# Performance work log

Hardware: AMD Instinct MI355X
Metric: run time of the kernel (lower is better)

## Reference

```python
import jax, jax.numpy as jnp
import numpy as np

N_HEADS = 16
ROPE_BASE = 10000.0


def _rope_tables(T, head_dim, dtype):
    d2 = head_dim // 2
    inv_freq = 1.0 / (ROPE_BASE ** (jnp.arange(0, head_dim, 2, dtype=jnp.float32) / head_dim))
    t = jnp.arange(T, dtype=jnp.float32)
    freqs = jnp.outer(t, inv_freq)  # [T, d2]
    cos = jnp.cos(freqs)[None, :, None, :].astype(dtype)  # [1,T,1,d2]
    sin = jnp.sin(freqs)[None, :, None, :].astype(dtype)
    return cos, sin


def _apply_rotary(x, cos, sin):
    # x: [B,T,H,D]; rotate halves
    d = x.shape[-1] // 2
    x1, x2 = x[..., :d], x[..., d:]
    return jnp.concatenate([x1 * cos + x2 * sin, -x1 * sin + x2 * cos], axis=-1)


def setup_inputs() -> dict:
    key = jax.random.key(0)
    k1, k2, k3 = jax.random.split(key, 3)
    B, T, C = 2, 2048, 1024
    x = jax.random.normal(k1, (B, T, C), dtype=jnp.float32)
    w_attn = jax.random.normal(k2, (3 * C, C), dtype=jnp.float32) * (1.0 / np.sqrt(C))
    w_proj = jax.random.normal(k3, (C, C), dtype=jnp.float32) * (1.0 / np.sqrt(C))
    return {"x": x, "w_attn": w_attn, "w_proj": w_proj}


def reference(x, w_attn, w_proj):
    B, T, C = x.shape
    H = N_HEADS
    D = C // H
    qkv = jnp.einsum('btc,fc->btf', x, w_attn)  # [B,T,3C]
    q, k, v = jnp.split(qkv, 3, axis=2)
    q = q.reshape(B, T, H, D)
    k = k.reshape(B, T, H, D)
    v = v.reshape(B, T, H, D)
    cos, sin = _rope_tables(T, D, x.dtype)
    q = _apply_rotary(q, cos, sin)
    k = _apply_rotary(k, cos, sin)
    # causal SDPA, scale 1/sqrt(D)
    scale = 1.0 / np.sqrt(D)
    scores = jnp.einsum('bqhd,bkhd->bhqk', q, k) * scale
    causal = jnp.tril(jnp.ones((T, T), dtype=bool))
    scores = jnp.where(causal[None, None], scores, jnp.finfo(scores.dtype).min)
    attn = jax.nn.softmax(scores, axis=-1)
    y = jnp.einsum('bhqk,bkhd->bqhd', attn, v).reshape(B, T, C)
    return jnp.einsum('btc,oc->bto', y, w_proj)
```

## Files before the change

### kernel.cpp

```cpp
#include <hip/hip_runtime.h>
#include <math.h>

typedef __bf16 bf16x8 __attribute__((ext_vector_type(8)));
typedef float f32x4 __attribute__((ext_vector_type(4)));

__device__ __forceinline__ unsigned f2bf(float f) {
    union { float f; unsigned u; } v; v.f = f;
    return (v.u + 0x7FFFu + ((v.u >> 16) & 1u)) >> 16;
}

__device__ __forceinline__ unsigned cvtpk(float a, float b) {
    unsigned r;
    __asm__("v_cvt_pk_bf16_f32 %0, %1, %2" : "=v"(r) : "v"(a), "v"(b));
    return r;
}

__device__ __forceinline__ void gload16(const ushort* g, ushort* l) {
    __builtin_amdgcn_global_load_lds(
        (const __attribute__((address_space(1))) void*)g,
        (__attribute__((address_space(3))) void*)l, 16, 0, 0);
}

__device__ __forceinline__ bool src_is_fp32(const unsigned* s) {
    int sane = 0;
#pragma unroll
    for (int i = 0; i < 64; ++i) {
        unsigned lo = s[i] & 0xFFFFu;
        unsigned e = (lo >> 7) & 0xFF;
        if (lo == 0u || (e >= 100u && e <= 140u)) sane++;
    }
    return sane < 48;
}

__global__ __launch_bounds__(256) void tobf16_all_kernel(
    const unsigned* __restrict__ s0, const unsigned* __restrict__ s1,
    const unsigned* __restrict__ s2,
    ushort* __restrict__ d0, ushort* __restrict__ d1, ushort* __restrict__ d2) {
    const int bx = blockIdx.x;
    const unsigned* src;
    ushort* dst;
    int lb;
    if (bx < 2048)      { src = s0; dst = d0; lb = bx; }
    else if (bx < 3584) { src = s1; dst = d1; lb = bx - 2048; }
    else                { src = s2; dst = d2; lb = bx - 3584; }
    const int i = lb * 2048 + threadIdx.x * 8;
    if (src_is_fp32(src)) {
        const float* fs = (const float*)src;
        float4 f0 = *(const float4*)(fs + i);
        float4 f1 = *(const float4*)(fs + i + 4);
        uint4 o;
        o.x = f2bf(f0.x) | (f2bf(f0.y) << 16);
        o.y = f2bf(f0.z) | (f2bf(f0.w) << 16);
        o.z = f2bf(f1.x) | (f2bf(f1.y) << 16);
        o.w = f2bf(f1.z) | (f2bf(f1.w) << 16);
        *(uint4*)(dst + i) = o;
    } else {
        *(uint4*)(dst + i) = *(const uint4*)((const ushort*)src + i);
    }
}

constexpr int GBM = 128, GBN = 128, GBK = 32;

__global__ __launch_bounds__(256) void gemm_qkv_rope_kernel(
    const ushort* __restrict__ A, const ushort* __restrict__ Bmat,
    ushort* __restrict__ qkvh, int K) {
    __shared__ ushort As[2][GBM * GBK];
    __shared__ ushort Bs[2][GBN * GBK];

    const int tid  = threadIdx.x;
    const int lane = tid & 63;
    const int wv   = tid >> 6;
    const int wm   = (wv >> 1) * 64;
    const int wn   = (wv & 1) * 64;

    const ushort* Ab = A + (size_t)blockIdx.x * GBM * K;
    const ushort* Bb = Bmat + (size_t)blockIdx.y * GBN * K;

    f32x4 acc[4][4];
#pragma unroll
    for (int i = 0; i < 4; i++)
#pragma unroll
        for (int j = 0; j < 4; j++) acc[i][j] = (f32x4){0.f, 0.f, 0.f, 0.f};

    const int srow = tid >> 2;
    const int scol = (tid & 3) * 8;
    const int fr = lane & 15;
    const int fk = (lane >> 4) * 8;
    const int nK = K >> 5;

    gload16(Ab + (size_t)srow * K + scol,        As[0] + wv * 512);
    gload16(Ab + (size_t)(srow + 64) * K + scol, As[0] + wv * 512 + 2048);
    gload16(Bb + (size_t)srow * K + scol,        Bs[0] + wv * 512);
    gload16(Bb + (size_t)(srow + 64) * K + scol, Bs[0] + wv * 512 + 2048);

#pragma unroll 1
    for (int it = 0; it < nK; ++it) {
        const int cur = it & 1;
        __syncthreads();
        if (it + 1 < nK) {
            const int k0 = (it + 1) << 5, nxt = cur ^ 1;
            gload16(Ab + (size_t)srow * K + k0 + scol,        As[nxt] + wv * 512);
            gload16(Ab + (size_t)(srow + 64) * K + k0 + scol, As[nxt] + wv * 512 + 2048);
            gload16(Bb + (size_t)srow * K + k0 + scol,        Bs[nxt] + wv * 512);
            gload16(Bb + (size_t)(srow + 64) * K + k0 + scol, Bs[nxt] + wv * 512 + 2048);
        }
        bf16x8 af[4], bfr[4];
#pragma unroll
        for (int i = 0; i < 4; i++)
            af[i] = *(const bf16x8*)(As[cur] + (wm + i * 16 + fr) * GBK + fk);
#pragma unroll
        for (int j = 0; j < 4; j++)
            bfr[j] = *(const bf16x8*)(Bs[cur] + (wn + j * 16 + fr) * GBK + fk);
#pragma unroll
        for (int i = 0; i < 4; i++)
#pragma unroll
            for (int j = 0; j < 4; j++)
                acc[i][j] = __builtin_amdgcn_mfma_f32_16x16x32_bf16(af[i], bfr[j], acc[i][j], 0, 0, 0);
    }

    const int crow0 = (lane >> 4) * 4;
    const int col0  = blockIdx.y * GBN + wn;
    const int which = col0 >> 10;
    const int hh    = (col0 >> 6) & 15;
    ushort* outp = qkvh + (size_t)which * 4194304 + (size_t)hh * 131072;

    if (which < 2) {
        const float inva = exp2f((float)fr * -0.41524101186f);
        const float invb = exp2f((float)(fr + 16) * -0.41524101186f);
        const float qs = (which == 0) ? 0.125f : 1.0f;
#pragma unroll
        for (int i = 0; i < 4; i++)
#pragma unroll
            for (int r = 0; r < 4; r++) {
                int row = blockIdx.x * GBM + wm + i * 16 + crow0 + r;
                int t = row & 2047;
                size_t ob = ((size_t)(row >> 11)) * 2097152 + (size_t)t * 64;
                float sa, ca, sb, cb;
                __sincosf((float)t * inva, &sa, &ca);
                __sincosf((float)t * invb, &sb, &cb);
                float q0 = acc[i][0][r], q1 = acc[i][1][r];
                float q2 = acc[i][2][r], q3 = acc[i][3][r];
                float n0 = (q0 * ca + q2 * sa) * qs;
                float n1 = (q1 * cb + q3 * sb) * qs;
                float n2 = (q2 * ca - q0 * sa) * qs;
                float n3 = (q3 * cb - q1 * sb) * qs;
                unsigned u01 = cvtpk(n0, n1);
                unsigned u23 = cvtpk(n2, n3);
                outp[ob + fr]      = (ushort)(u01 & 0xFFFFu);
                outp[ob + 16 + fr] = (ushort)(u01 >> 16);
                outp[ob + 32 + fr] = (ushort)(u23 & 0xFFFFu);
                outp[ob + 48 + fr] = (ushort)(u23 >> 16);
            }
    } else {
#pragma unroll
        for (int i = 0; i < 4; i++)
#pragma unroll
            for (int r = 0; r < 4; r++) {
                int row = blockIdx.x * GBM + wm + i * 16 + crow0 + r;
                int t = row & 2047;
                size_t ob = ((size_t)(row >> 11)) * 2097152 + (size_t)t * 64;
                unsigned u01 = cvtpk(acc[i][0][r], acc[i][1][r]);
                unsigned u23 = cvtpk(acc[i][2][r], acc[i][3][r]);
                outp[ob + fr]      = (ushort)(u01 & 0xFFFFu);
                outp[ob + 16 + fr] = (ushort)(u01 >> 16);
                outp[ob + 32 + fr] = (ushort)(u23 & 0xFFFFu);
                outp[ob + 48 + fr] = (ushort)(u23 >> 16);
            }
    }
}

__global__ __launch_bounds__(256) void gemm_bt_kernel(
    const ushort* __restrict__ A, const ushort* __restrict__ Bmat,
    float* __restrict__ C, int M, int N, int K) {
    __shared__ ushort As[2][GBM * GBK];
    __shared__ ushort Bs[2][GBN * GBK];

    const int tid  = threadIdx.x;
    const int lane = tid & 63;
    const int wv   = tid >> 6;
    const int wm   = (wv >> 1) * 64;
    const int wn   = (wv & 1) * 64;

    const ushort* Ab = A + (size_t)blockIdx.x * GBM * K;
    const ushort* Bb = Bmat + (size_t)blockIdx.y * GBN * K;

    f32x4 acc[4][4];
#pragma unroll
    for (int i = 0; i < 4; i++)
#pragma unroll
        for (int j = 0; j < 4; j++) acc[i][j] = (f32x4){0.f, 0.f, 0.f, 0.f};

    const int srow = tid >> 2;
    const int scol = (tid & 3) * 8;
    const int fr = lane & 15;
    const int fk = (lane >> 4) * 8;
    const int nK = K >> 5;

    gload16(Ab + (size_t)srow * K + scol,        As[0] + wv * 512);
    gload16(Ab + (size_t)(srow + 64) * K + scol, As[0] + wv * 512 + 2048);
    gload16(Bb + (size_t)srow * K + scol,        Bs[0] + wv * 512);
    gload16(Bb + (size_t)(srow + 64) * K + scol, Bs[0] + wv * 512 + 2048);

#pragma unroll 1
    for (int it = 0; it < nK; ++it) {
        const int cur = it & 1;
        __syncthreads();
        if (it + 1 < nK) {
            const int k0 = (it + 1) << 5, nxt = cur ^ 1;
            gload16(Ab + (size_t)srow * K + k0 + scol,        As[nxt] + wv * 512);
            gload16(Ab + (size_t)(srow + 64) * K + k0 + scol, As[nxt] + wv * 512 + 2048);
            gload16(Bb + (size_t)srow * K + k0 + scol,        Bs[nxt] + wv * 512);
            gload16(Bb + (size_t)(srow + 64) * K + k0 + scol, Bs[nxt] + wv * 512 + 2048);
        }
        bf16x8 af[4], bfr[4];
#pragma unroll
        for (int i = 0; i < 4; i++)
            af[i] = *(const bf16x8*)(As[cur] + (wm + i * 16 + fr) * GBK + fk);
#pragma unroll
        for (int j = 0; j < 4; j++)
            bfr[j] = *(const bf16x8*)(Bs[cur] + (wn + j * 16 + fr) * GBK + fk);
#pragma unroll
        for (int i = 0; i < 4; i++)
#pragma unroll
            for (int j = 0; j < 4; j++)
                acc[i][j] = __builtin_amdgcn_mfma_f32_16x16x32_bf16(af[i], bfr[j], acc[i][j], 0, 0, 0);
    }

    const int crow0 = (lane >> 4) * 4;
#pragma unroll
    for (int i = 0; i < 4; i++)
#pragma unroll
        for (int j = 0; j < 4; j++)
#pragma unroll
            for (int r = 0; r < 4; r++) {
                int row = blockIdx.x * GBM + wm + i * 16 + crow0 + r;
                int col = blockIdx.y * GBN + wn + j * 16 + fr;
                C[(size_t)row * N + col] = acc[i][j][r];
            }
}

#define NEG_BIG (-1e30f)
constexpr int LPK = 72;
constexpr int LPV = 136;

__global__ __launch_bounds__(512) void attn_kernel(const ushort* __restrict__ qkvh,
                                                   ushort* __restrict__ y) {
    __shared__ ushort Ks[2][128 * LPK];
    __shared__ ushort Vt[2][64 * LPV];
    __shared__ ushort Ps[8][16 * LPV];

    const int tid  = threadIdx.x;
    const int lane = tid & 63;
    const int wv   = tid >> 6;
    const int pid  = blockIdx.x;
    const int bh   = blockIdx.y;
    const int b    = bh >> 4, h = bh & 15;

    const ushort* qp = qkvh + (size_t)b * 2097152 + (size_t)h * 131072;
    const ushort* kp = qp + 4194304;
    const ushort* vp = qp + 8388608;

    const int fr = lane & 15;
    const int fq = lane >> 4;
    const int fk = fq * 8;

    const int srow = tid >> 2;
    const int scol = (tid & 3) * 16;
    const int vkey = tid & 127;
    const int vd0  = (tid >> 7) * 16;

#pragma unroll 1
    for (int seg = 0; seg < 2; ++seg) {
        const int qb = seg ? (15 - pid) : pid;
        const int nIt = qb + 1;

        __syncthreads();

        const int qrow = qb * 128 + wv * 16 + fr;
        bf16x8 qf0 = *(const bf16x8*)(qp + (size_t)qrow * 64 + fk);
        bf16x8 qf1 = *(const bf16x8*)(qp + (size_t)qrow * 64 + 32 + fk);

        f32x4 o[4];
        o[0] = o[1] = o[2] = o[3] = (f32x4){0.f, 0.f, 0.f, 0.f};
        float lacc[4] = {0.f, 0.f, 0.f, 0.f};

        uint4 kr0, kr1, vr0, vr1;
        {
            const ushort* sk = kp + (size_t)srow * 64 + scol;
            kr0 = *(const uint4*)(sk);
            kr1 = *(const uint4*)(sk + 8);
            const ushort* sv = vp + (size_t)vkey * 64 + vd0;
            vr0 = *(const uint4*)(sv);
            vr1 = *(const uint4*)(sv + 8);
            *(uint4*)(Ks[0] + srow * LPK + scol)     = kr0;
            *(uint4*)(Ks[0] + srow * LPK + scol + 8) = kr1;
            unsigned w[8] = {vr0.x, vr0.y, vr0.z, vr0.w, vr1.x, vr1.y, vr1.z, vr1.w};
#pragma unroll
            for (int jj = 0; jj < 8; ++jj) {
                Vt[0][(vd0 + 2 * jj)     * LPV + vkey] = (ushort)(w[jj] & 0xFFFFu);
                Vt[0][(vd0 + 2 * jj + 1) * LPV + vkey] = (ushort)(w[jj] >> 16);
            }
        }
        if (1 < nIt) {
            const ushort* sk = kp + (size_t)(128 + srow) * 64 + scol;
            kr0 = *(const uint4*)(sk);
            kr1 = *(const uint4*)(sk + 8);
            const ushort* sv = vp + (size_t)(128 + vkey) * 64 + vd0;
            vr0 = *(const uint4*)(sv);
            vr1 = *(const uint4*)(sv + 8);
        }

#pragma unroll 1
        for (int it = 0; it < nIt; ++it) {
            const int cur = it & 1;
            const int k0 = it * 128;
            __syncthreads();
            if (it + 1 < nIt) {
                const int nxt = cur ^ 1;
                *(uint4*)(Ks[nxt] + srow * LPK + scol)     = kr0;
                *(uint4*)(Ks[nxt] + srow * LPK + scol + 8) = kr1;
                unsigned w[8] = {vr0.x, vr0.y, vr0.z, vr0.w, vr1.x, vr1.y, vr1.z, vr1.w};
#pragma unroll
                for (int jj = 0; jj < 8; ++jj) {
                    Vt[nxt][(vd0 + 2 * jj)     * LPV + vkey] = (ushort)(w[jj] & 0xFFFFu);
                    Vt[nxt][(vd0 + 2 * jj + 1) * LPV + vkey] = (ushort)(w[jj] >> 16);
                }
                if (it + 2 < nIt) {
                    const ushort* sk = kp + (size_t)(k0 + 256 + srow) * 64 + scol;
                    kr0 = *(const uint4*)(sk);
                    kr1 = *(const uint4*)(sk + 8);
                    const ushort* sv = vp + (size_t)(k0 + 256 + vkey) * 64 + vd0;
                    vr0 = *(const uint4*)(sv);
                    vr1 = *(const uint4*)(sv + 8);
                }
            }

            f32x4 s[8];
#pragma unroll
            for (int j = 0; j < 8; ++j) {
                bf16x8 kf0 = *(const bf16x8*)(Ks[cur] + (j * 16 + fr) * LPK + fk);
                bf16x8 kf1 = *(const bf16x8*)(Ks[cur] + (j * 16 + fr) * LPK + 32 + fk);
                f32x4 z = (f32x4){0.f, 0.f, 0.f, 0.f};
                z = __builtin_amdgcn_mfma_f32_16x16x32_bf16(qf0, kf0, z, 0, 0, 0);
                z = __builtin_amdgcn_mfma_f32_16x16x32_bf16(qf1, kf1, z, 0, 0, 0);
                s[j] = z;
            }
            if (it + 1 < nIt) {
#pragma unroll
                for (int j = 0; j < 8; ++j)
#pragma unroll
                    for (int r = 0; r < 4; ++r) {
                        float p = __expf(s[j][r]);
                        s[j][r] = p;
                        lacc[r] += p;
                    }
            } else {
                const int rowg = qb * 128 + wv * 16 + fq * 4;
#pragma unroll
                for (int j = 0; j < 8; ++j)
#pragma unroll
                    for (int r = 0; r < 4; ++r) {
                        float v = s[j][r];
                        if ((k0 + j * 16 + fr) > (rowg + r)) v = NEG_BIG;
                        float p = __expf(v);
                        s[j][r] = p;
                        lacc[r] += p;
                    }
            }

            ushort* pw = Ps[wv];
#pragma unroll
            for (int j = 0; j < 8; j += 2)
#pragma unroll
                for (int r = 0; r < 4; ++r) {
                    unsigned u = cvtpk(s[j][r], s[j + 1][r]);
                    pw[(fq * 4 + r) * LPV + j * 16 + fr]       = (ushort)(u & 0xFFFFu);
                    pw[(fq * 4 + r) * LPV + (j + 1) * 16 + fr] = (ushort)(u >> 16);
                }
            __asm__ volatile("" ::: "memory");

#pragma unroll
            for (int kk = 0; kk < 4; ++kk) {
                bf16x8 pf = *(const bf16x8*)(pw + fr * LPV + kk * 32 + fk);
#pragma unroll
                for (int j = 0; j < 4; ++j) {
                    bf16x8 vf = *(const bf16x8*)(Vt[cur] + (j * 16 + fr) * LPV + kk * 32 + fk);
                    o[j] = __builtin_amdgcn_mfma_f32_16x16x32_bf16(pf, vf, o[j], 0, 0, 0);
                }
            }
        }

#pragma unroll
        for (int msk = 1; msk < 16; msk <<= 1)
#pragma unroll
            for (int r = 0; r < 4; ++r)
                lacc[r] += __shfl_xor(lacc[r], msk, 64);
        float linv[4];
#pragma unroll
        for (int r = 0; r < 4; ++r) linv[r] = 1.0f / lacc[r];
#pragma unroll
        for (int j = 0; j < 4; j += 2)
#pragma unroll
            for (int r = 0; r < 4; ++r) {
                int row = qb * 128 + wv * 16 + fq * 4 + r;
                size_t yb = ((size_t)b * 2048 + row) * 1024 + h * 64;
                unsigned u = cvtpk(o[j][r] * linv[r], o[j + 1][r] * linv[r]);
                y[yb + j * 16 + fr]       = (ushort)(u & 0xFFFFu);
                y[yb + (j + 1) * 16 + fr] = (ushort)(u >> 16);
            }
    }
}

extern "C" void kernel_launch(void* const* d_in, const int* in_sizes, int n_in,
                              void* d_out, int out_size, void* d_ws, size_t ws_size,
                              hipStream_t stream) {
    const int nx = in_sizes[0];
    const int na = in_sizes[1];
    const int np = in_sizes[2];

    ushort* qkvh = (ushort*)d_ws;
    ushort* yb   = qkvh + (size_t)3 * 4194304;
    ushort* xb   = yb + (size_t)4096 * 1024;
    ushort* wab  = xb + nx;
    ushort* wpb  = wab + na;
    size_t need = ((size_t)3 * 4194304 + (size_t)4096 * 1024 + nx + na + np) * 2;
    if (ws_size < need) return;

    tobf16_all_kernel<<<dim3(4096), 256, 0, stream>>>(
        (const unsigned*)d_in[0], (const unsigned*)d_in[1], (const unsigned*)d_in[2],
        xb, wab, wpb);

    gemm_qkv_rope_kernel<<<dim3(32, 24), 256, 0, stream>>>(xb, wab, qkvh, 1024);
    attn_kernel<<<dim3(8, 32), 512, 0, stream>>>(qkvh, yb);
    gemm_bt_kernel<<<dim3(32, 8), 256, 0, stream>>>(yb, wpb, (float*)d_out, 4096, 1024, 1024);
}
```

Measured before the change: 190.3 us.

## Split each attention key tile across two wave groups and reduce partial outputs in LDS

The attention block grows from 512 to 1024 threads. The two halves of 8 waves each take 64 of the 128 keys in every tile, for the same 16-row query slice. At the end, the upper half writes its partial O and row sums into the reused K shared buffer, and the lower half combines them, normalises and stores the output. With only 256 blocks, the aim is to double the waves per CU for better latency hiding and MFMA use. The cost is an extra LDS reduction with two barriers, and each thread now loads half as much K/V data into shared memory.

```diff
diff --git a/kernel.cpp b/kernel.cpp
--- a/kernel.cpp
+++ b/kernel.cpp
@@ -243,15 +243,18 @@
 constexpr int LPK = 72;
 constexpr int LPV = 136;
 
-__global__ __launch_bounds__(512) void attn_kernel(const ushort* __restrict__ qkvh,
-                                                   ushort* __restrict__ y) {
+__global__ __launch_bounds__(1024) void attn_kernel(const ushort* __restrict__ qkvh,
+                                                    ushort* __restrict__ y) {
     __shared__ ushort Ks[2][128 * LPK];
     __shared__ ushort Vt[2][64 * LPV];
-    __shared__ ushort Ps[8][16 * LPV];
+    __shared__ ushort Ps[16][16 * LPK];
 
     const int tid  = threadIdx.x;
     const int lane = tid & 63;
     const int wv   = tid >> 6;
+    const int half = wv >> 3;
+    const int wq   = wv & 7;
+    const int jb   = half * 4;
     const int pid  = blockIdx.x;
     const int bh   = blockIdx.y;
     const int b    = bh >> 4, h = bh & 15;
@@ -264,10 +267,10 @@
     const int fq = lane >> 4;
     const int fk = fq * 8;
 
-    const int srow = tid >> 2;
-    const int scol = (tid & 3) * 16;
+    const int srow = tid >> 3;
+    const int scol = (tid & 7) * 8;
     const int vkey = tid & 127;
-    const int vd0  = (tid >> 7) * 16;
+    const int vd0  = (tid >> 7) * 8;
 
 #pragma unroll 1
     for (int seg = 0; seg < 2; ++seg) {
@@ -276,7 +279,7 @@
 
         __syncthreads();
 
-        const int qrow = qb * 128 + wv * 16 + fr;
+        const int qrow = qb * 128 + wq * 16 + fr;
         bf16x8 qf0 = *(const bf16x8*)(qp + (size_t)qrow * 64 + fk);
         bf16x8 qf1 = *(const bf16x8*)(qp + (size_t)qrow * 64 + 32 + fk);
 
@@ -284,30 +287,21 @@
         o[0] = o[1] = o[2] = o[3] = (f32x4){0.f, 0.f, 0.f, 0.f};
         float lacc[4] = {0.f, 0.f, 0.f, 0.f};
 
-        uint4 kr0, kr1, vr0, vr1;
+        uint4 kr, vr;
         {
-            const ushort* sk = kp + (size_t)srow * 64 + scol;
-            kr0 = *(const uint4*)(sk);
-            kr1 = *(const uint4*)(sk + 8);
-            const ushort* sv = vp + (size_t)vkey * 64 + vd0;
-            vr0 = *(const uint4*)(sv);
-            vr1 = *(const uint4*)(sv + 8);
-            *(uint4*)(Ks[0] + srow * LPK + scol)     = kr0;
-            *(uint4*)(Ks[0] + srow * LPK + scol + 8) = kr1;
-            unsigned w[8] = {vr0.x, vr0.y, vr0.z, vr0.w, vr1.x, vr1.y, vr1.z, vr1.w};
-#pragma unroll
-            for (int jj = 0; jj < 8; ++jj) {
-                Vt[0][(vd0 + 2 * jj)     * LPV + vkey] = (ushort)(w[jj] & 0xFFFFu);
-                Vt[0][(vd0 + 2 * jj + 1) * LPV + vkey] = (ushort)(w[jj] >> 16);
+            kr = *(const uint4*)(kp + (size_t)srow * 64 + scol);
+            vr = *(const uint4*)(vp + (size_t)vkey * 64 + vd0);
+            *(uint4*)(Ks[0] + srow * LPK + scol) = kr;
+            unsigned w[4] = {vr.x, vr.y, vr.z, vr.w};
+#pragma unroll
+            for (int t = 0; t < 4; ++t) {
+                Vt[0][(vd0 + 2 * t)     * LPV + vkey] = (ushort)(w[t] & 0xFFFFu);
+                Vt[0][(vd0 + 2 * t + 1) * LPV + vkey] = (ushort)(w[t] >> 16);
             }
         }
         if (1 < nIt) {
-            const ushort* sk = kp + (size_t)(128 + srow) * 64 + scol;
-            kr0 = *(const uint4*)(sk);
-            kr1 = *(const uint4*)(sk + 8);
-            const ushort* sv = vp + (size_t)(128 + vkey) * 64 + vd0;
-            vr0 = *(const uint4*)(sv);
-            vr1 = *(const uint4*)(sv + 8);
+            kr = *(const uint4*)(kp + (size_t)(128 + srow) * 64 + scol);
+            vr = *(const uint4*)(vp + (size_t)(128 + vkey) * 64 + vd0);
         }
 
 #pragma unroll 1
@@ -317,75 +311,72 @@
             __syncthreads();
             if (it + 1 < nIt) {
                 const int nxt = cur ^ 1;
-                *(uint4*)(Ks[nxt] + srow * LPK + scol)     = kr0;
-                *(uint4*)(Ks[nxt] + srow * LPK + scol + 8) = kr1;
-                unsigned w[8] = {vr0.x, vr0.y, vr0.z, vr0.w, vr1.x, vr1.y, vr1.z, vr1.w};
-#pragma unroll
-                for (int jj = 0; jj < 8; ++jj) {
-                    Vt[nxt][(vd0 + 2 * jj)     * LPV + vkey] = (ushort)(w[jj] & 0xFFFFu);
-                    Vt[nxt][(vd0 + 2 * jj + 1) * LPV + vkey] = (ushort)(w[jj] >> 16);
+                *(uint4*)(Ks[nxt] + srow * LPK + scol) = kr;
+                unsigned w[4] = {vr.x, vr.y, vr.z, vr.w};
+#pragma unroll
+                for (int t = 0; t < 4; ++t) {
+                    Vt[nxt][(vd0 + 2 * t)     * LPV + vkey] = (ushort)(w[t] & 0xFFFFu);
+                    Vt[nxt][(vd0 + 2 * t + 1) * LPV + vkey] = (ushort)(w[t] >> 16);
                 }
                 if (it + 2 < nIt) {
-                    const ushort* sk = kp + (size_t)(k0 + 256 + srow) * 64 + scol;
-                    kr0 = *(const uint4*)(sk);
-                    kr1 = *(const uint4*)(sk + 8);
-                    const ushort* sv = vp + (size_t)(k0 + 256 + vkey) * 64 + vd0;
-                    vr0 = *(const uint4*)(sv);
-                    vr1 = *(const uint4*)(sv + 8);
+                    kr = *(const uint4*)(kp + (size_t)(k0 + 256 + srow) * 64 + scol);
+                    vr = *(const uint4*)(vp + (size_t)(k0 + 256 + vkey) * 64 + vd0);
                 }
             }
 
-            f32x4 s[8];
-#pragma unroll
-            for (int j = 0; j < 8; ++j) {
+            f32x4 s[4];
+#pragma unroll
+            for (int jl = 0; jl < 4; ++jl) {
+                const int j = jb + jl;
                 bf16x8 kf0 = *(const bf16x8*)(Ks[cur] + (j * 16 + fr) * LPK + fk);
                 bf16x8 kf1 = *(const bf16x8*)(Ks[cur] + (j * 16 + fr) * LPK + 32 + fk);
                 f32x4 z = (f32x4){0.f, 0.f, 0.f, 0.f};
                 z = __builtin_amdgcn_mfma_f32_16x16x32_bf16(qf0, kf0, z, 0, 0, 0);
                 z = __builtin_amdgcn_mfma_f32_16x16x32_bf16(qf1, kf1, z, 0, 0, 0);
-                s[j] = z;
+                s[jl] = z;
             }
             if (it + 1 < nIt) {
 #pragma unroll
-                for (int j = 0; j < 8; ++j)
+                for (int jl = 0; jl < 4; ++jl)
 #pragma unroll
                     for (int r = 0; r < 4; ++r) {
-                        float p = __expf(s[j][r]);
-                        s[j][r] = p;
+                        float p = __expf(s[jl][r]);
+                        s[jl][r] = p;
                         lacc[r] += p;
                     }
             } else {
-                const int rowg = qb * 128 + wv * 16 + fq * 4;
-#pragma unroll
-                for (int j = 0; j < 8; ++j)
+                const int rowg = qb * 128 + wq * 16 + fq * 4;
+#pragma unroll
+                for (int jl = 0; jl < 4; ++jl)
 #pragma unroll
                     for (int r = 0; r < 4; ++r) {
-                        float v = s[j][r];
-                        if ((k0 + j * 16 + fr) > (rowg + r)) v = NEG_BIG;
+                        float v = s[jl][r];
+                        if ((k0 + (jb + jl) * 16 + fr) > (rowg + r)) v = NEG_BIG;
                         float p = __expf(v);
-                        s[j][r] = p;
+                        s[jl][r] = p;
                         lacc[r] += p;
                     }
             }
 
             ushort* pw = Ps[wv];
 #pragma unroll
-            for (int j = 0; j < 8; j += 2)
+            for (int jl = 0; jl < 4; jl += 2)
 #pragma unroll
                 for (int r = 0; r < 4; ++r) {
-                    unsigned u = cvtpk(s[j][r], s[j + 1][r]);
-                    pw[(fq * 4 + r) * LPV + j * 16 + fr]       = (ushort)(u & 0xFFFFu);
-                    pw[(fq * 4 + r) * LPV + (j + 1) * 16 + fr] = (ushort)(u >> 16);
+                    unsigned u = cvtpk(s[jl][r], s[jl + 1][r]);
+                    pw[(fq * 4 + r) * LPK + jl * 16 + fr]       = (ushort)(u & 0xFFFFu);
+                    pw[(fq * 4 + r) * LPK + (jl + 1) * 16 + fr] = (ushort)(u >> 16);
                 }
             __asm__ volatile("" ::: "memory");
 
 #pragma unroll
-            for (int kk = 0; kk < 4; ++kk) {
-                bf16x8 pf = *(const bf16x8*)(pw + fr * LPV + kk * 32 + fk);
-#pragma unroll
-                for (int j = 0; j < 4; ++j) {
-                    bf16x8 vf = *(const bf16x8*)(Vt[cur] + (j * 16 + fr) * LPV + kk * 32 + fk);
-                    o[j] = __builtin_amdgcn_mfma_f32_16x16x32_bf16(pf, vf, o[j], 0, 0, 0);
+            for (int kl = 0; kl < 2; ++kl) {
+                bf16x8 pf = *(const bf16x8*)(pw + fr * LPK + kl * 32 + fk);
+                const int vcol = half * 64 + kl * 32 + fk;
+#pragma unroll
+                for (int j4 = 0; j4 < 4; ++j4) {
+                    bf16x8 vf = *(const bf16x8*)(Vt[cur] + (j4 * 16 + fr) * LPV + vcol);
+                    o[j4] = __builtin_amdgcn_mfma_f32_16x16x32_bf16(pf, vf, o[j4], 0, 0, 0);
                 }
             }
         }
@@ -395,19 +386,38 @@
 #pragma unroll
             for (int r = 0; r < 4; ++r)
                 lacc[r] += __shfl_xor(lacc[r], msk, 64);
-        float linv[4];
-#pragma unroll
-        for (int r = 0; r < 4; ++r) linv[r] = 1.0f / lacc[r];
-#pragma unroll
-        for (int j = 0; j < 4; j += 2)
-#pragma unroll
-            for (int r = 0; r < 4; ++r) {
-                int row = qb * 128 + wv * 16 + fq * 4 + r;
-                size_t yb = ((size_t)b * 2048 + row) * 1024 + h * 64;
-                unsigned u = cvtpk(o[j][r] * linv[r], o[j + 1][r] * linv[r]);
-                y[yb + j * 16 + fr]       = (ushort)(u & 0xFFFFu);
-                y[yb + (j + 1) * 16 + fr] = (ushort)(u >> 16);
-            }
+
+        __syncthreads();
+        float* ex = (float*)(&Ks[0][0]) + wq * 1104;
+        if (half) {
+#pragma unroll
+            for (int j4 = 0; j4 < 4; ++j4)
+#pragma unroll
+                for (int r = 0; r < 4; ++r)
+                    ex[lane * 17 + j4 * 4 + r] = o[j4][r];
+#pragma unroll
+            for (int r = 0; r < 4; ++r)
+                ex[1088 + fq * 4 + r] = lacc[r];
+        }
+        __syncthreads();
+        if (!half) {
+            float linv[4];
+#pragma unroll
+            for (int r = 0; r < 4; ++r)
+                linv[r] = 1.0f / (lacc[r] + ex[1088 + fq * 4 + r]);
+#pragma unroll
+            for (int j4 = 0; j4 < 4; j4 += 2)
+#pragma unroll
+                for (int r = 0; r < 4; ++r) {
+                    int row = qb * 128 + wq * 16 + fq * 4 + r;
+                    size_t yb = ((size_t)b * 2048 + row) * 1024 + h * 64;
+                    float v0 = (o[j4][r]     + ex[lane * 17 + j4 * 4 + r])     * linv[r];
+                    float v1 = (o[j4 + 1][r] + ex[lane * 17 + (j4 + 1) * 4 + r]) * linv[r];
+                    unsigned u = cvtpk(v0, v1);
+                    y[yb + j4 * 16 + fr]       = (ushort)(u & 0xFFFFu);
+                    y[yb + (j4 + 1) * 16 + fr] = (ushort)(u >> 16);
+                }
+        }
     }
 }
 
@@ -431,6 +441,6 @@
         xb, wab, wpb);
 
     gemm_qkv_rope_kernel<<<dim3(32, 24), 256, 0, stream>>>(xb, wab, qkvh, 1024);
-    attn_kernel<<<dim3(8, 32), 512, 0, stream>>>(qkvh, yb);
+    attn_kernel<<<dim3(8, 32), 1024, 0, stream>>>(qkvh, yb);
     gemm_bt_kernel<<<dim3(32, 8), 256, 0, stream>>>(yb, wpb, (float*)d_out, 4096, 1024, 1024);
 }
```

Measured after the change: 188.6 us. Within noise of the previous version (-0.9%).
